# Kernel optimization log

Measured on AMD Instinct MI355X. Metric: run time of the kernel, lower is better.

The kernel has to match this reference:

```python
import jax, jax.numpy as jnp
import numpy as np

N_NODES = 50000
N_EDGES = 1600000
NEG_SLOPE = 0.2


def setup_inputs() -> dict:
    key = jax.random.key(0)
    ks = jax.random.split(key, 11)
    s = 0.1  # small init scale
    return {
        "x": jax.random.normal(ks[0], (N_NODES, 128), dtype=jnp.float32),
        "edge_index": jax.random.randint(ks[1], (2, N_EDGES), 0, N_NODES, dtype=jnp.int64),
        "W1": jax.random.normal(ks[2], (128, 128), dtype=jnp.float32) * s,
        "att_src1": jax.random.normal(ks[3], (2, 64), dtype=jnp.float32) * s,
        "att_dst1": jax.random.normal(ks[4], (2, 64), dtype=jnp.float32) * s,
        "b1": jax.random.normal(ks[5], (128,), dtype=jnp.float32) * s,
        "W2": jax.random.normal(ks[6], (128, 64), dtype=jnp.float32) * s,
        "att_src2": jax.random.normal(ks[7], (1, 64), dtype=jnp.float32) * s,
        "att_dst2": jax.random.normal(ks[8], (1, 64), dtype=jnp.float32) * s,
        "b2": jax.random.normal(ks[9], (64,), dtype=jnp.float32) * s,
    }


def gat_conv(x, W, a_src, a_dst, bias, src, dst, n_nodes):
    # x: [N, F_in]; W: [F_in, H*C]; a_src/a_dst: [H, C]; bias: [H*C]
    H, C = a_src.shape
    xl = (x @ W).reshape(n_nodes, H, C)                 # [N,H,C]
    alpha_s = jnp.einsum('nhc,hc->nh', xl, a_src)       # [N,H]
    alpha_d = jnp.einsum('nhc,hc->nh', xl, a_dst)       # [N,H]
    e = jax.nn.leaky_relu(alpha_s[src] + alpha_d[dst], NEG_SLOPE)  # [E,H]
    # segment softmax over edges sharing the same destination node
    m = jax.ops.segment_max(e, dst, num_segments=n_nodes)          # [N,H]
    m = jnp.where(jnp.isfinite(m), m, 0.0)
    e = jnp.exp(e - m[dst])
    denom = jax.ops.segment_sum(e, dst, num_segments=n_nodes)      # [N,H]
    alpha = e / denom[dst]                               # self-loops guarantee denom > 0
    msg = xl[src] * alpha[:, :, None]                    # [E,H,C]
    out = jax.ops.segment_sum(msg, dst, num_segments=n_nodes)      # [N,H,C]
    return out.reshape(n_nodes, H * C) + bias


def reference(x, edge_index, W1, att_src1, att_dst1, b1, W2, att_src2, att_dst2, b2):
    n = x.shape[0]
    # PyG GATConv default add_self_loops=True
    loops = jnp.arange(n, dtype=edge_index.dtype)
    src = jnp.concatenate([edge_index[0], loops])
    dst = jnp.concatenate([edge_index[1], loops])

    h = gat_conv(x, W1, att_src1, att_dst1, b1, src, dst, n)   # [N, 128]
    h = jax.nn.relu(h)                                          # dropout p=0 (eval)
    h = gat_conv(h, W2, att_src2, att_dst2, b2, src, dst, n)   # [N, 64]
    h = jax.nn.relu(h)
    return h
```

## Files before the change

kernel.cpp:

```cpp
#include <hip/hip_runtime.h>
#include <hip/hip_fp16.h>
#include <cstdint>
#include <cstddef>

#define NEG_SLOPE 0.2f

#define NB 128
#define LOG_NB 7
#define MAXK 512

__device__ inline unsigned short f2bf(float f) {
    unsigned int u = __float_as_uint(f);
    u += 0x7FFFu + ((u >> 16) & 1u);
    return (unsigned short)(u >> 16);
}
__device__ inline float bf_lo(unsigned int u) { return __uint_as_float(u << 16); }
__device__ inline float bf_hi(unsigned int u) { return __uint_as_float(u & 0xFFFF0000u); }
__device__ inline float bfu(unsigned short u) { return __uint_as_float((unsigned int)u << 16); }
__device__ inline float lrelu(float t) { return t > 0.f ? t : NEG_SLOPE * t; }

#define FMA8(a, v)                                                                       \
    acc[0] = fmaf(a, bf_lo((v).x), acc[0]); acc[1] = fmaf(a, bf_hi((v).x), acc[1]);      \
    acc[2] = fmaf(a, bf_lo((v).y), acc[2]); acc[3] = fmaf(a, bf_hi((v).y), acc[3]);      \
    acc[4] = fmaf(a, bf_lo((v).z), acc[4]); acc[5] = fmaf(a, bf_hi((v).z), acc[5]);      \
    acc[6] = fmaf(a, bf_lo((v).w), acc[6]); acc[7] = fmaf(a, bf_hi((v).w), acc[7]);

__global__ __launch_bounds__(256) void sort_count_kernel(const int* __restrict__ ei, int E,
                                                         int K, int CH, int* __restrict__ bcnt) {
    __shared__ int hist[4 * MAXK];
    int tid = threadIdx.x;
    int wiw = tid >> 6;
    for (int i = tid; i < K; i += 256) {
        hist[i] = 0; hist[MAXK + i] = 0; hist[2 * MAXK + i] = 0; hist[3 * MAXK + i] = 0;
    }
    __syncthreads();
    int lo = blockIdx.x * CH;
    int hi = lo + CH; if (hi > E) hi = E;
    for (int e = lo + tid; e < hi; e += 256)
        atomicAdd(&hist[wiw * MAXK + (ei[(size_t)E + e] >> LOG_NB)], 1);
    __syncthreads();
    for (int i = tid; i < K; i += 256) {
        int c = hist[i] + hist[MAXK + i] + hist[2 * MAXK + i] + hist[3 * MAXK + i];
        if (c) atomicAdd(&bcnt[i], c);
    }
}

__global__ void sort_scan_kernel(const int* __restrict__ bcnt, int* __restrict__ boff,
                                 int* __restrict__ bcur, int K, int E) {
    __shared__ int buf[MAXK];
    int tid = threadIdx.x;
    int v = (tid < K) ? bcnt[tid] : 0;
    buf[tid] = v;
    __syncthreads();
    for (int o = 1; o < MAXK; o <<= 1) {
        int t = (tid >= o) ? buf[tid - o] : 0;
        __syncthreads();
        buf[tid] += t;
        __syncthreads();
    }
    if (tid < K) {
        int ex = buf[tid] - v;
        boff[tid] = ex;
        bcur[tid] = ex;
    }
    if (tid == K) boff[K] = E;
}


template <int FOUT, int H, int ROWS, bool BF16IN, bool CHUNK_OUT>
__device__ __forceinline__ void gemm_att_body(const void* __restrict__ Xv,
                                              const float* __restrict__ W,
                                              const float* __restrict__ attS,
                                              const float* __restrict__ attD,
                                              unsigned short* __restrict__ Ybf,
                                              float* __restrict__ as_,
                                              float* __restrict__ ad_, int N, int bid,
                                              float* sX, float* sW) {
    constexpr int CG  = FOUT / 4;
    constexpr int RR  = (ROWS * FOUT) / 1024;
    constexpr int LDX = 36;
    int tid = threadIdx.x;
    int rowbase = bid * ROWS;
    int cg = tid % CG;
    int rg = tid / CG;
    int r0 = rg * RR;

    float acc[RR][4];
#pragma unroll
    for (int i = 0; i < RR; i++)
#pragma unroll
        for (int c = 0; c < 4; c++) acc[i][c] = 0.f;

    for (int k0 = 0; k0 < 128; k0 += 32) {
        __syncthreads();
        for (int idx = tid; idx < ROWS * 8; idx += 256) {
            int r = idx >> 3, q = idx & 7;
            int row = rowbase + r;
            float4 val;
            if (row < N) {
                if constexpr (BF16IN) {
                    const unsigned short* Xb = (const unsigned short*)Xv;
                    ushort4 raw = *(const ushort4*)&Xb[(size_t)row * 128 + k0 + q * 4];
                    val = make_float4(bfu(raw.x), bfu(raw.y), bfu(raw.z), bfu(raw.w));
                } else {
                    const float* X = (const float*)Xv;
                    val = *(const float4*)&X[(size_t)row * 128 + k0 + q * 4];
                }
            } else {
                val = make_float4(0.f, 0.f, 0.f, 0.f);
            }
            *(float4*)&sX[r * LDX + q * 4] = val;
        }
        for (int idx = tid; idx < 8 * FOUT; idx += 256)
            *(float4*)&sW[idx * 4] = *(const float4*)&W[(size_t)k0 * FOUT + idx * 4];
        __syncthreads();
        for (int k = 0; k < 32; k += 4) {
            float4 xr[RR];
#pragma unroll
            for (int i = 0; i < RR; i++)
                xr[i] = *(const float4*)&sX[(r0 + i) * LDX + k];
#pragma unroll
            for (int kk = 0; kk < 4; kk++) {
                float4 wv = ((const float4*)(sW + (size_t)(k + kk) * FOUT))[cg];
#pragma unroll
                for (int i = 0; i < RR; i++) {
                    float xv = (&xr[i].x)[kk];
                    acc[i][0] = fmaf(xv, wv.x, acc[i][0]);
                    acc[i][1] = fmaf(xv, wv.y, acc[i][1]);
                    acc[i][2] = fmaf(xv, wv.z, acc[i][2]);
                    acc[i][3] = fmaf(xv, wv.w, acc[i][3]);
                }
            }
        }
    }

#pragma unroll
    for (int i = 0; i < RR; i++) {
        int row = rowbase + r0 + i;
        if (row < N) {
            ushort4 v;
            v.x = f2bf(acc[i][0]); v.y = f2bf(acc[i][1]);
            v.z = f2bf(acc[i][2]); v.w = f2bf(acc[i][3]);
            if constexpr (CHUNK_OUT) {
                int chunk = cg >> 3;
                int wc = (cg & 7) * 4;
                *(ushort4*)(Ybf + ((size_t)chunk * N + row) * 32 + wc) = v;
            } else {
                *(ushort4*)(Ybf + (size_t)row * FOUT + cg * 4) = v;
            }
        }
    }

    float4 asv = ((const float4*)attS)[cg];
    float4 adv = ((const float4*)attD)[cg];
    int head = (H == 2) ? (cg >> 4) : 0;
#pragma unroll
    for (int i = 0; i < RR; i++) {
        float ps = acc[i][0] * asv.x + acc[i][1] * asv.y + acc[i][2] * asv.z + acc[i][3] * asv.w;
        float pd = acc[i][0] * adv.x + acc[i][1] * adv.y + acc[i][2] * adv.z + acc[i][3] * adv.w;
#pragma unroll
        for (int o = 1; o <= 8; o <<= 1) { ps += __shfl_xor(ps, o); pd += __shfl_xor(pd, o); }
        int row = rowbase + r0 + i;
        if ((tid & 15) == 0 && row < N) {
            as_[(size_t)row * H + head] = ps;
            ad_[(size_t)row * H + head] = pd;
        }
    }
}

__global__ __launch_bounds__(256) void scatter_gemm1_kernel(const int* __restrict__ ei, int E,
                                                            int K, int CH, int* __restrict__ bcur,
                                                            unsigned int* __restrict__ bkt,
                                                            const float* __restrict__ X,
                                                            const float* __restrict__ W1,
                                                            const float* __restrict__ attS,
                                                            const float* __restrict__ attD,
                                                            unsigned short* __restrict__ Ybf,
                                                            float* __restrict__ as_,
                                                            float* __restrict__ ad_, int N, int G) {
    __shared__ float sX[64 * 36];
    __shared__ float sW[32 * 128];
    if (blockIdx.x < G) {
        int* hist = (int*)sX;
        int* base = (int*)sW;
        int* cur2 = (int*)sW + MAXK;
        int tid = threadIdx.x;
        int wiw = tid >> 6;
        for (int i = tid; i < K; i += 256) {
            hist[i] = 0; hist[MAXK + i] = 0; hist[2 * MAXK + i] = 0; hist[3 * MAXK + i] = 0;
        }
        __syncthreads();
        int lo = blockIdx.x * CH;
        int hi = lo + CH; if (hi > E) hi = E;
        for (int e = lo + tid; e < hi; e += 256)
            atomicAdd(&hist[wiw * MAXK + (ei[(size_t)E + e] >> LOG_NB)], 1);
        __syncthreads();
        for (int i = tid; i < K; i += 256) {
            int c = hist[i] + hist[MAXK + i] + hist[2 * MAXK + i] + hist[3 * MAXK + i];
            base[i] = c ? atomicAdd(&bcur[i], c) : 0;
            cur2[i] = 0;
        }
        __syncthreads();
        for (int e = lo + tid; e < hi; e += 256) {
            int s = ei[e];
            int d = ei[(size_t)E + e];
            int k = d >> LOG_NB;
            int r = atomicAdd(&cur2[k], 1);
            bkt[(size_t)base[k] + r] = (unsigned int)s | ((unsigned int)d << 16);
        }
    } else {
        gemm_att_body<128, 2, 64, false, true>(X, W1, attS, attD, Ybf, as_, ad_, N,
                                               blockIdx.x - G, sX, sW);
    }
}

__global__ __launch_bounds__(256) void gemm2_kernel(const unsigned short* __restrict__ X,
                                                    const float* __restrict__ W,
                                                    const float* __restrict__ attS,
                                                    const float* __restrict__ attD,
                                                    unsigned short* __restrict__ Ybf,
                                                    float* __restrict__ as_,
                                                    float* __restrict__ ad_, int N) {
    __shared__ float sX[64 * 36];
    __shared__ float sW[32 * 64];
    gemm_att_body<64, 1, 64, true, false>(X, W, attS, attD, Ybf, as_, ad_, N, blockIdx.x, sX, sW);
}


__global__ __launch_bounds__(256) void sort_finalize_kernel(const unsigned int* __restrict__ bkt,
                                                            const int* __restrict__ boff,
                                                            int* __restrict__ off,
                                                            unsigned int* __restrict__ csrc,
                                                            const float* __restrict__ as_,
                                                            const float* __restrict__ ad_,
                                                            unsigned int* __restrict__ pae0,
                                                            unsigned int* __restrict__ pae1,
                                                            int N) {
    __shared__ int nhist[4 * NB];
    __shared__ int part[256];
    __shared__ int loff[NB];
    int k = blockIdx.x;
    int tid = threadIdx.x;
    int wiw = tid >> 6;
    int node0 = k << LOG_NB;
    int nh = N - node0; if (nh > NB) nh = NB;
    int beg = boff[k], end = boff[k + 1];
    for (int i = tid; i < NB; i += 256) {
        nhist[i] = 0; nhist[NB + i] = 0; nhist[2 * NB + i] = 0; nhist[3 * NB + i] = 0;
    }
    __syncthreads();
    for (int e = beg + tid; e < end; e += 256)
        atomicAdd(&nhist[wiw * NB + ((bkt[e] >> 16) - node0)], 1);
    __syncthreads();
    int i0 = 2 * tid, i1 = 2 * tid + 1;
    int v0 = (i0 < nh) ? nhist[i0] + nhist[NB + i0] + nhist[2 * NB + i0] + nhist[3 * NB + i0] + 1 : 0;
    int v1 = (i1 < nh) ? nhist[i1] + nhist[NB + i1] + nhist[2 * NB + i1] + nhist[3 * NB + i1] + 1 : 0;
    part[tid] = v0 + v1;
    __syncthreads();
    for (int o = 1; o < 256; o <<= 1) {
        int t = (tid >= o) ? part[tid - o] : 0;
        __syncthreads();
        part[tid] += t;
        __syncthreads();
    }
    int gbase = beg + node0;
    int base = gbase + ((tid > 0) ? part[tid - 1] : 0);
    if (i0 < nh) loff[i0] = base;
    if (i1 < nh) loff[i1] = base + v0;
    __syncthreads();
    for (int i = tid; i < nh; i += 256) {
        int node = node0 + i;
        off[node] = loff[i];
        csrc[loff[i]] = (unsigned int)node | ((unsigned int)node << 16);
        nhist[i] = loff[i] + 1;
    }
    if (node0 + nh == N && tid == 0) off[N] = gbase + part[255];
    __syncthreads();
    for (int e = beg + tid; e < end; e += 256) {
        unsigned int p = bkt[e];
        int pos = atomicAdd(&nhist[(p >> 16) - node0], 1);
        csrc[pos] = p;
    }
    __syncthreads();

    int lane = tid & 63;
    for (int i = wiw; i < nh; i += 4) {
        int node = node0 + i;
        int nb = loff[i];
        int ne = nhist[i];
        int deg = ne - nb;
        float2 adn = ((const float2*)ad_)[node];

        if (deg <= 64) {
            int s = 0;
            float t0 = -1e30f, t1 = -1e30f;
            if (lane < deg) {
                s = (int)(csrc[nb + lane] & 0xFFFFu);
                float2 asv = ((const float2*)as_)[s];
                t0 = lrelu(asv.x + adn.x);
                t1 = lrelu(asv.y + adn.y);
            }
            float m0 = t0, m1 = t1;
#pragma unroll
            for (int o = 32; o; o >>= 1) {
                m0 = fmaxf(m0, __shfl_xor(m0, o));
                m1 = fmaxf(m1, __shfl_xor(m1, o));
            }
            float e0 = (lane < deg) ? __expf(t0 - m0) : 0.f;
            float e1 = (lane < deg) ? __expf(t1 - m1) : 0.f;
            float s0 = e0, s1 = e1;
#pragma unroll
            for (int o = 32; o; o >>= 1) { s0 += __shfl_xor(s0, o); s1 += __shfl_xor(s1, o); }
            if (lane < deg) {
                unsigned int h0 = (unsigned int)__half_as_ushort(__float2half(e0 / s0));
                unsigned int h1 = (unsigned int)__half_as_ushort(__float2half(e1 / s1));
                pae0[nb + lane] = (unsigned int)s | (h0 << 16);
                pae1[nb + lane] = (unsigned int)s | (h1 << 16);
            }
        } else {
            float m0 = -1e30f, m1 = -1e30f;
            for (int b = nb; b < ne; b += 64) {
                int e = b + lane;
                if (e < ne) {
                    int s = (int)(csrc[e] & 0xFFFFu);
                    float2 asv = ((const float2*)as_)[s];
                    m0 = fmaxf(m0, lrelu(asv.x + adn.x));
                    m1 = fmaxf(m1, lrelu(asv.y + adn.y));
                }
            }
#pragma unroll
            for (int o = 32; o; o >>= 1) {
                m0 = fmaxf(m0, __shfl_xor(m0, o));
                m1 = fmaxf(m1, __shfl_xor(m1, o));
            }
            float s0 = 0.f, s1 = 0.f;
            for (int b = nb; b < ne; b += 64) {
                int e = b + lane;
                if (e < ne) {
                    int s = (int)(csrc[e] & 0xFFFFu);
                    float2 asv = ((const float2*)as_)[s];
                    s0 += __expf(lrelu(asv.x + adn.x) - m0);
                    s1 += __expf(lrelu(asv.y + adn.y) - m1);
                }
            }
#pragma unroll
            for (int o = 32; o; o >>= 1) { s0 += __shfl_xor(s0, o); s1 += __shfl_xor(s1, o); }
            float i0r = 1.f / s0, i1r = 1.f / s1;
            for (int b = nb; b < ne; b += 64) {
                int e = b + lane;
                if (e < ne) {
                    int s = (int)(csrc[e] & 0xFFFFu);
                    float2 asv = ((const float2*)as_)[s];
                    float a0 = __expf(lrelu(asv.x + adn.x) - m0) * i0r;
                    float a1 = __expf(lrelu(asv.y + adn.y) - m1) * i1r;
                    unsigned int h0 = (unsigned int)__half_as_ushort(__float2half(a0));
                    unsigned int h1 = (unsigned int)__half_as_ushort(__float2half(a1));
                    pae0[e] = (unsigned int)s | (h0 << 16);
                    pae1[e] = (unsigned int)s | (h1 << 16);
                }
            }
        }
    }
}


__global__ __launch_bounds__(256) void chunk_agg1_kernel(const unsigned short* __restrict__ xlc,
                                                         const unsigned int* __restrict__ pae0,
                                                         const unsigned int* __restrict__ pae1,
                                                         const float* __restrict__ bias,
                                                         const int* __restrict__ off,
                                                         unsigned short* __restrict__ out,
                                                         int N) {
    int bid   = blockIdx.x;
    int slot  = bid & 7;
    int chunk = slot & 3;
    int half  = slot >> 2;
    int blkin = (bid >> 3) * 2 + half;
    int wiw   = threadIdx.x >> 6;
    int lane  = threadIdx.x & 63;
    int node  = blkin * 16 + wiw * 4 + (lane >> 4);
    int l16   = lane & 15;
    int esub  = l16 >> 2;
    int li    = l16 & 3;

    bool valid = node < N;
    int beg = 0, deg = 0;
    if (valid) { beg = off[node]; deg = off[node + 1] - beg; }

    int md = deg;
    md = max(md, __shfl_xor(md, 16));
    md = max(md, __shfl_xor(md, 32));
    int iters = (md + 3) >> 2;

    const unsigned int* pae = (chunk & 2) ? pae1 : pae0;
    const char* xb = (const char*)xlc + ((size_t)chunk * N) * 64 + li * 16;

    float acc[8];
#pragma unroll
    for (int i = 0; i < 8; i++) acc[i] = 0.f;

#pragma unroll 2
    for (int r = 0; r < iters; r++) {
        int e = r * 4 + esub;
        unsigned int p = (e < deg) ? pae[beg + e] : 0u;
        float a = __half2float(__ushort_as_half((unsigned short)(p >> 16)));
        int s = (int)(p & 0xFFFFu);
        uint4 v = *(const uint4*)(xb + ((size_t)s << 6));
        FMA8(a, v)
    }
#pragma unroll
    for (int o = 4; o <= 8; o <<= 1)
#pragma unroll
        for (int i = 0; i < 8; i++) acc[i] += __shfl_xor(acc[i], o);

    if (valid && esub == 0) {
        const float* bp = bias + chunk * 32 + li * 8;
        unsigned int w0 = (unsigned int)f2bf(fmaxf(acc[0] + bp[0], 0.f)) |
                          ((unsigned int)f2bf(fmaxf(acc[1] + bp[1], 0.f)) << 16);
        unsigned int w1 = (unsigned int)f2bf(fmaxf(acc[2] + bp[2], 0.f)) |
                          ((unsigned int)f2bf(fmaxf(acc[3] + bp[3], 0.f)) << 16);
        unsigned int w2 = (unsigned int)f2bf(fmaxf(acc[4] + bp[4], 0.f)) |
                          ((unsigned int)f2bf(fmaxf(acc[5] + bp[5], 0.f)) << 16);
        unsigned int w3 = (unsigned int)f2bf(fmaxf(acc[6] + bp[6], 0.f)) |
                          ((unsigned int)f2bf(fmaxf(acc[7] + bp[7], 0.f)) << 16);
        *(uint4*)(out + (size_t)node * 128 + chunk * 32 + li * 8) = make_uint4(w0, w1, w2, w3);
    }
}


__global__ __launch_bounds__(256) void agg2_kernel(const unsigned short* __restrict__ xl,
                                                   const float* __restrict__ as_,
                                                   const float* __restrict__ ad_,
                                                   const float* __restrict__ bias,
                                                   const int* __restrict__ off,
                                                   const unsigned int* __restrict__ csrc,
                                                   float* __restrict__ out, int N) {
    __shared__ float2 sps[4][64];
    int wiw  = threadIdx.x >> 6;
    int lane = threadIdx.x & 63;
    int node = blockIdx.x * 4 + wiw;
    if (node >= N) return;
    int beg = off[node], end = off[node + 1];
    int deg = end - beg;
    float adn = ad_[node];

    int cl  = lane & 7;
    int sub = lane >> 3;
    float acc[8];
#pragma unroll
    for (int i = 0; i < 8; i++) acc[i] = 0.f;
    const char* xbase = (const char*)xl + cl * 16;

    if (deg <= 64) {
        int so = 0;
        float t = -1e30f;
        if (lane < deg) {
            int s = (int)(csrc[beg + lane] & 0xFFFFu);
            so = s << 7;
            t = as_[s] + adn;
            t = t > 0.f ? t : NEG_SLOPE * t;
        }
        float m = t;
#pragma unroll
        for (int o = 32; o; o >>= 1) m = fmaxf(m, __shfl_xor(m, o));
        float evv = (lane < deg) ? __expf(t - m) : 0.f;
        float sum = evv;
#pragma unroll
        for (int o = 32; o; o >>= 1) sum += __shfl_xor(sum, o);
        sps[wiw][lane] = make_float2(evv / sum, __int_as_float(so));
        int iters = (deg + 7) >> 3;
        int g = 0;
        for (; g + 4 <= iters; g += 4) {
            float2 q0 = sps[wiw][(g + 0) * 8 + sub];
            float2 q1 = sps[wiw][(g + 1) * 8 + sub];
            float2 q2 = sps[wiw][(g + 2) * 8 + sub];
            float2 q3 = sps[wiw][(g + 3) * 8 + sub];
            uint4 v0 = *(const uint4*)(xbase + __float_as_int(q0.y));
            uint4 v1 = *(const uint4*)(xbase + __float_as_int(q1.y));
            uint4 v2 = *(const uint4*)(xbase + __float_as_int(q2.y));
            uint4 v3 = *(const uint4*)(xbase + __float_as_int(q3.y));
            FMA8(q0.x, v0) FMA8(q1.x, v1) FMA8(q2.x, v2) FMA8(q3.x, v3)
        }
        for (; g < iters; g++) {
            float2 q = sps[wiw][g * 8 + sub];
            uint4 v  = *(const uint4*)(xbase + __float_as_int(q.y));
            FMA8(q.x, v)
        }
    } else {
        float m = -1e30f;
        for (int b = beg; b < end; b += 64) {
            int e = b + lane;
            if (e < end) {
                float t = as_[csrc[e] & 0xFFFFu] + adn;
                t = t > 0.f ? t : NEG_SLOPE * t;
                m = fmaxf(m, t);
            }
        }
#pragma unroll
        for (int o = 32; o; o >>= 1) m = fmaxf(m, __shfl_xor(m, o));
        float sum = 0.f;
        for (int b = beg; b < end; b += 64) {
            int e = b + lane;
            if (e < end) {
                float t = as_[csrc[e] & 0xFFFFu] + adn;
                t = t > 0.f ? t : NEG_SLOPE * t;
                sum += __expf(t - m);
            }
        }
#pragma unroll
        for (int o = 32; o; o >>= 1) sum += __shfl_xor(sum, o);
        float inv = 1.f / sum;
        for (int b = beg; b < end; b += 64) {
            int cnt = end - b; if (cnt > 64) cnt = 64;
            float p = 0.f; int so = 0;
            if (lane < cnt) {
                int s = (int)(csrc[b + lane] & 0xFFFFu);
                so = s << 7;
                float t = as_[s] + adn;
                t = t > 0.f ? t : NEG_SLOPE * t;
                p = __expf(t - m) * inv;
            }
            sps[wiw][lane] = make_float2(p, __int_as_float(so));
            int iters = (cnt + 7) >> 3;
#pragma unroll 8
            for (int j = 0; j < iters; j++) {
                float2 q = sps[wiw][j * 8 + sub];
                float a  = q.x;
                uint4 v  = *(const uint4*)(xbase + __float_as_int(q.y));
                FMA8(a, v)
            }
        }
    }
#pragma unroll
    for (int o = 8; o <= 32; o <<= 1)
#pragma unroll
        for (int i = 0; i < 8; i++) acc[i] += __shfl_xor(acc[i], o);
    if (sub == 0) {
        float* op = out + (size_t)node * 64 + cl * 8;
        const float* bp = bias + cl * 8;
#pragma unroll
        for (int i = 0; i < 8; i++) op[i] = fmaxf(acc[i] + bp[i], 0.f);
    }
}


extern "C" void kernel_launch(void* const* d_in, const int* in_sizes, int n_in,
                              void* d_out, int out_size, void* d_ws, size_t ws_size,
                              hipStream_t stream) {
    const float* x        = (const float*)d_in[0];
    const int*   ei       = (const int*)d_in[1];
    const float* W1       = (const float*)d_in[2];
    const float* attS1    = (const float*)d_in[3];
    const float* attD1    = (const float*)d_in[4];
    const float* b1       = (const float*)d_in[5];
    const float* W2       = (const float*)d_in[6];
    const float* attS2    = (const float*)d_in[7];
    const float* attD2    = (const float*)d_in[8];
    const float* b2       = (const float*)d_in[9];
    float* out            = (float*)d_out;

    int N  = in_sizes[0] / 128;
    int E  = in_sizes[1] / 2;
    int EE = E + N;
    int K  = (N + NB - 1) >> LOG_NB;

    char* w = (char*)d_ws;
    auto alloc = [&](size_t bytes) -> void* {
        void* p = (void*)w;
        w += (bytes + 255) & ~(size_t)255;
        return p;
    };
    int*   bcnt = (int*)alloc((size_t)(K + 1) * 4);
    int*   boff = (int*)alloc((size_t)(K + 1) * 4);
    int*   bcur = (int*)alloc((size_t)(K + 1) * 4);
    int*   off  = (int*)alloc((size_t)(N + 1) * 4);
    unsigned int* csrc = (unsigned int*)alloc((size_t)EE * 4);
    unsigned int* bkt  = (unsigned int*)alloc((size_t)E * 4);
    unsigned short* xl1 = (unsigned short*)alloc((size_t)N * 128 * 2);
    float* sd1  = (float*)alloc((size_t)N * 2 * 4);
    float* dd1  = (float*)alloc((size_t)N * 2 * 4);
    unsigned short* h1 = (unsigned short*)alloc((size_t)N * 128 * 2);
    unsigned int* pae0 = (unsigned int*)alloc((size_t)EE * 4);
    unsigned int* pae1 = (unsigned int*)alloc((size_t)EE * 4);

    unsigned short* xl2 = xl1;
    float* sd2 = sd1;
    float* dd2 = dd1;

    hipMemsetAsync(bcnt, 0, (size_t)(K + 1) * 4, stream);

    int G   = 256;
    int CH  = (E + G - 1) / G;
    int GB1 = (N + 63) / 64;
    sort_count_kernel<<<G, 256, 0, stream>>>(ei, E, K, CH, bcnt);
    sort_scan_kernel<<<1, MAXK, 0, stream>>>(bcnt, boff, bcur, K, E);
    scatter_gemm1_kernel<<<G + GB1, 256, 0, stream>>>(ei, E, K, CH, bcur, bkt,
                                                      x, W1, attS1, attD1, xl1, sd1, dd1, N, G);
    sort_finalize_kernel<<<K, 256, 0, stream>>>(bkt, boff, off, csrc, sd1, dd1, pae0, pae1, N);

    int NG  = (N + 15) / 16;
    int CAB = ((NG + 1) / 2) * 8;
    chunk_agg1_kernel<<<CAB, 256, 0, stream>>>(xl1, pae0, pae1, b1, off, h1, N);

    gemm2_kernel<<<(N + 63) / 64, 256, 0, stream>>>(h1, W2, attS2, attD2, xl2, sd2, dd2, N);
    agg2_kernel<<<(N + 3) / 4, 256, 0, stream>>>(xl2, sd2, dd2, b2, off, csrc, out, N);
}
```

Measured before the change: 308.0 us.

## Fuse layer-1 edge softmax into aggregation and drop precomputed attention arrays

```diff
diff --git a/kernel.cpp b/kernel.cpp
--- a/kernel.cpp
+++ b/kernel.cpp
@@ -1,5 +1,4 @@
 #include <hip/hip_runtime.h>
-#include <hip/hip_fp16.h>
 #include <cstdint>
 #include <cstddef>
 
@@ -17,7 +16,6 @@
 __device__ inline float bf_lo(unsigned int u) { return __uint_as_float(u << 16); }
 __device__ inline float bf_hi(unsigned int u) { return __uint_as_float(u & 0xFFFF0000u); }
 __device__ inline float bfu(unsigned short u) { return __uint_as_float((unsigned int)u << 16); }
-__device__ inline float lrelu(float t) { return t > 0.f ? t : NEG_SLOPE * t; }
 
 #define FMA8(a, v)                                                                       \
     acc[0] = fmaf(a, bf_lo((v).x), acc[0]); acc[1] = fmaf(a, bf_hi((v).x), acc[1]);      \
@@ -226,16 +224,10 @@
     gemm_att_body<64, 1, 64, true, false>(X, W, attS, attD, Ybf, as_, ad_, N, blockIdx.x, sX, sW);
 }
 
-
 __global__ __launch_bounds__(256) void sort_finalize_kernel(const unsigned int* __restrict__ bkt,
                                                             const int* __restrict__ boff,
                                                             int* __restrict__ off,
-                                                            unsigned int* __restrict__ csrc,
-                                                            const float* __restrict__ as_,
-                                                            const float* __restrict__ ad_,
-                                                            unsigned int* __restrict__ pae0,
-                                                            unsigned int* __restrict__ pae1,
-                                                            int N) {
+                                                            unsigned int* __restrict__ csrc, int N) {
     __shared__ int nhist[4 * NB];
     __shared__ int part[256];
     __shared__ int loff[NB];
@@ -281,92 +273,13 @@
         int pos = atomicAdd(&nhist[(p >> 16) - node0], 1);
         csrc[pos] = p;
     }
-    __syncthreads();
-
-    int lane = tid & 63;
-    for (int i = wiw; i < nh; i += 4) {
-        int node = node0 + i;
-        int nb = loff[i];
-        int ne = nhist[i];
-        int deg = ne - nb;
-        float2 adn = ((const float2*)ad_)[node];
-
-        if (deg <= 64) {
-            int s = 0;
-            float t0 = -1e30f, t1 = -1e30f;
-            if (lane < deg) {
-                s = (int)(csrc[nb + lane] & 0xFFFFu);
-                float2 asv = ((const float2*)as_)[s];
-                t0 = lrelu(asv.x + adn.x);
-                t1 = lrelu(asv.y + adn.y);
-            }
-            float m0 = t0, m1 = t1;
-#pragma unroll
-            for (int o = 32; o; o >>= 1) {
-                m0 = fmaxf(m0, __shfl_xor(m0, o));
-                m1 = fmaxf(m1, __shfl_xor(m1, o));
-            }
-            float e0 = (lane < deg) ? __expf(t0 - m0) : 0.f;
-            float e1 = (lane < deg) ? __expf(t1 - m1) : 0.f;
-            float s0 = e0, s1 = e1;
-#pragma unroll
-            for (int o = 32; o; o >>= 1) { s0 += __shfl_xor(s0, o); s1 += __shfl_xor(s1, o); }
-            if (lane < deg) {
-                unsigned int h0 = (unsigned int)__half_as_ushort(__float2half(e0 / s0));
-                unsigned int h1 = (unsigned int)__half_as_ushort(__float2half(e1 / s1));
-                pae0[nb + lane] = (unsigned int)s | (h0 << 16);
-                pae1[nb + lane] = (unsigned int)s | (h1 << 16);
-            }
-        } else {
-            float m0 = -1e30f, m1 = -1e30f;
-            for (int b = nb; b < ne; b += 64) {
-                int e = b + lane;
-                if (e < ne) {
-                    int s = (int)(csrc[e] & 0xFFFFu);
-                    float2 asv = ((const float2*)as_)[s];
-                    m0 = fmaxf(m0, lrelu(asv.x + adn.x));
-                    m1 = fmaxf(m1, lrelu(asv.y + adn.y));
-                }
-            }
-#pragma unroll
-            for (int o = 32; o; o >>= 1) {
-                m0 = fmaxf(m0, __shfl_xor(m0, o));
-                m1 = fmaxf(m1, __shfl_xor(m1, o));
-            }
-            float s0 = 0.f, s1 = 0.f;
-            for (int b = nb; b < ne; b += 64) {
-                int e = b + lane;
-                if (e < ne) {
-                    int s = (int)(csrc[e] & 0xFFFFu);
-                    float2 asv = ((const float2*)as_)[s];
-                    s0 += __expf(lrelu(asv.x + adn.x) - m0);
-                    s1 += __expf(lrelu(asv.y + adn.y) - m1);
-                }
-            }
-#pragma unroll
-            for (int o = 32; o; o >>= 1) { s0 += __shfl_xor(s0, o); s1 += __shfl_xor(s1, o); }
-            float i0r = 1.f / s0, i1r = 1.f / s1;
-            for (int b = nb; b < ne; b += 64) {
-                int e = b + lane;
-                if (e < ne) {
-                    int s = (int)(csrc[e] & 0xFFFFu);
-                    float2 asv = ((const float2*)as_)[s];
-                    float a0 = __expf(lrelu(asv.x + adn.x) - m0) * i0r;
-                    float a1 = __expf(lrelu(asv.y + adn.y) - m1) * i1r;
-                    unsigned int h0 = (unsigned int)__half_as_ushort(__float2half(a0));
-                    unsigned int h1 = (unsigned int)__half_as_ushort(__float2half(a1));
-                    pae0[e] = (unsigned int)s | (h0 << 16);
-                    pae1[e] = (unsigned int)s | (h1 << 16);
-                }
-            }
-        }
-    }
 }
 
 
 __global__ __launch_bounds__(256) void chunk_agg1_kernel(const unsigned short* __restrict__ xlc,
-                                                         const unsigned int* __restrict__ pae0,
-                                                         const unsigned int* __restrict__ pae1,
+                                                         const unsigned int* __restrict__ csrc,
+                                                         const float* __restrict__ as_,
+                                                         const float* __restrict__ ad_,
                                                          const float* __restrict__ bias,
                                                          const int* __restrict__ off,
                                                          unsigned short* __restrict__ out,
@@ -382,47 +295,60 @@
     int l16   = lane & 15;
     int esub  = l16 >> 2;
     int li    = l16 & 3;
+    int hc    = chunk >> 1;
 
     bool valid = node < N;
     int beg = 0, deg = 0;
-    if (valid) { beg = off[node]; deg = off[node + 1] - beg; }
+    float adn = 0.f;
+    if (valid) {
+        beg = off[node];
+        deg = off[node + 1] - beg;
+        adn = ad_[node * 2 + hc];
+    }
 
     int md = deg;
     md = max(md, __shfl_xor(md, 16));
     md = max(md, __shfl_xor(md, 32));
     int iters = (md + 3) >> 2;
 
-    const unsigned int* pae = (chunk & 2) ? pae1 : pae0;
     const char* xb = (const char*)xlc + ((size_t)chunk * N) * 64 + li * 16;
 
     float acc[8];
+    float wsum = 0.f;
 #pragma unroll
     for (int i = 0; i < 8; i++) acc[i] = 0.f;
 
 #pragma unroll 2
     for (int r = 0; r < iters; r++) {
         int e = r * 4 + esub;
-        unsigned int p = (e < deg) ? pae[beg + e] : 0u;
-        float a = __half2float(__ushort_as_half((unsigned short)(p >> 16)));
+        bool act = e < deg;
+        unsigned int p = act ? csrc[beg + e] : 0u;
         int s = (int)(p & 0xFFFFu);
+        float t = as_[s * 2 + hc] + adn;
+        t = t > 0.f ? t : NEG_SLOPE * t;
+        float w = act ? __expf(t) : 0.f;
         uint4 v = *(const uint4*)(xb + ((size_t)s << 6));
-        FMA8(a, v)
-    }
-#pragma unroll
-    for (int o = 4; o <= 8; o <<= 1)
+        wsum += w;
+        FMA8(w, v)
+    }
+#pragma unroll
+    for (int o = 4; o <= 8; o <<= 1) {
+        wsum += __shfl_xor(wsum, o);
 #pragma unroll
         for (int i = 0; i < 8; i++) acc[i] += __shfl_xor(acc[i], o);
+    }
 
     if (valid && esub == 0) {
+        float inv = 1.f / wsum;
         const float* bp = bias + chunk * 32 + li * 8;
-        unsigned int w0 = (unsigned int)f2bf(fmaxf(acc[0] + bp[0], 0.f)) |
-                          ((unsigned int)f2bf(fmaxf(acc[1] + bp[1], 0.f)) << 16);
-        unsigned int w1 = (unsigned int)f2bf(fmaxf(acc[2] + bp[2], 0.f)) |
-                          ((unsigned int)f2bf(fmaxf(acc[3] + bp[3], 0.f)) << 16);
-        unsigned int w2 = (unsigned int)f2bf(fmaxf(acc[4] + bp[4], 0.f)) |
-                          ((unsigned int)f2bf(fmaxf(acc[5] + bp[5], 0.f)) << 16);
-        unsigned int w3 = (unsigned int)f2bf(fmaxf(acc[6] + bp[6], 0.f)) |
-                          ((unsigned int)f2bf(fmaxf(acc[7] + bp[7], 0.f)) << 16);
+        unsigned int w0 = (unsigned int)f2bf(fmaxf(fmaf(acc[0], inv, bp[0]), 0.f)) |
+                          ((unsigned int)f2bf(fmaxf(fmaf(acc[1], inv, bp[1]), 0.f)) << 16);
+        unsigned int w1 = (unsigned int)f2bf(fmaxf(fmaf(acc[2], inv, bp[2]), 0.f)) |
+                          ((unsigned int)f2bf(fmaxf(fmaf(acc[3], inv, bp[3]), 0.f)) << 16);
+        unsigned int w2 = (unsigned int)f2bf(fmaxf(fmaf(acc[4], inv, bp[4]), 0.f)) |
+                          ((unsigned int)f2bf(fmaxf(fmaf(acc[5], inv, bp[5]), 0.f)) << 16);
+        unsigned int w3 = (unsigned int)f2bf(fmaxf(fmaf(acc[6], inv, bp[6]), 0.f)) |
+                          ((unsigned int)f2bf(fmaxf(fmaf(acc[7], inv, bp[7]), 0.f)) << 16);
         *(uint4*)(out + (size_t)node * 128 + chunk * 32 + li * 8) = make_uint4(w0, w1, w2, w3);
     }
 }
@@ -580,8 +506,6 @@
     float* sd1  = (float*)alloc((size_t)N * 2 * 4);
     float* dd1  = (float*)alloc((size_t)N * 2 * 4);
     unsigned short* h1 = (unsigned short*)alloc((size_t)N * 128 * 2);
-    unsigned int* pae0 = (unsigned int*)alloc((size_t)EE * 4);
-    unsigned int* pae1 = (unsigned int*)alloc((size_t)EE * 4);
 
     unsigned short* xl2 = xl1;
     float* sd2 = sd1;
@@ -596,11 +520,11 @@
     sort_scan_kernel<<<1, MAXK, 0, stream>>>(bcnt, boff, bcur, K, E);
     scatter_gemm1_kernel<<<G + GB1, 256, 0, stream>>>(ei, E, K, CH, bcur, bkt,
                                                       x, W1, attS1, attD1, xl1, sd1, dd1, N, G);
-    sort_finalize_kernel<<<K, 256, 0, stream>>>(bkt, boff, off, csrc, sd1, dd1, pae0, pae1, N);
+    sort_finalize_kernel<<<K, 256, 0, stream>>>(bkt, boff, off, csrc, N);
 
     int NG  = (N + 15) / 16;
     int CAB = ((NG + 1) / 2) * 8;
-    chunk_agg1_kernel<<<CAB, 256, 0, stream>>>(xl1, pae0, pae1, b1, off, h1, N);
+    chunk_agg1_kernel<<<CAB, 256, 0, stream>>>(xl1, csrc, sd1, dd1, b1, off, h1, N);
 
     gemm2_kernel<<<(N + 63) / 64, 256, 0, stream>>>(h1, W2, attS2, attD2, xl2, sd2, dd2, N);
     agg2_kernel<<<(N + 3) / 4, 256, 0, stream>>>(xl2, sd2, dd2, b2, off, csrc, out, N);
```

New measurement: 297.7 us. -3.3%, faster.
